# Kernel tuning notes

Hardware: AMD Instinct MI355X
Metric: run time of the kernel (lower is better)

Reference implementation:

```python
import jax, jax.numpy as jnp
import numpy as np

N, E, DIN, DH, DOUT, G = 100000, 1600000, 128, 128, 40, 512


def setup_inputs() -> dict:
    key = jax.random.key(0)
    ks = jax.random.split(key, 8)
    x = jax.random.normal(ks[0], (N, DIN), dtype=jnp.float32)
    src = jax.random.randint(ks[1], (E,), 0, N)
    dst = jax.random.randint(ks[2], (E,), 0, N)
    batch = jnp.sort(jax.random.randint(ks[3], (N,), 0, G))
    W1 = jax.random.normal(ks[4], (DIN, DH), dtype=jnp.float32) * (1.0 / np.sqrt(DIN))
    b1 = jnp.zeros((DH,), dtype=jnp.float32)
    W2 = jax.random.normal(ks[5], (DH, DOUT), dtype=jnp.float32) * (1.0 / np.sqrt(DH))
    b2 = jnp.zeros((DOUT,), dtype=jnp.float32)
    return {"x": x, "src": src, "dst": dst, "batch": batch,
            "W1": W1, "b1": b1, "W2": W2, "b2": b2, "num_graphs": G}


def gcn_conv(h, src, dst, n, W, b):
    # PyG GCNConv: linear transform, then D^-1/2 (A + I) D^-1/2 aggregation.
    h = h @ W  # [n, d_out]
    # degree on destination nodes, including self-loop weight 1
    deg = jax.ops.segment_sum(jnp.ones_like(dst, dtype=h.dtype), dst, num_segments=n) + 1.0
    dinv = jax.lax.rsqrt(deg)  # deg >= 1 so always finite
    coef = dinv[src] * dinv[dst]  # [E]
    agg = jax.ops.segment_sum(h[src] * coef[:, None], dst, num_segments=n)
    agg = agg + h * (dinv * dinv)[:, None]  # self-loop term
    return agg + b


def reference(x, src, dst, batch, W1, b1, W2, b2, num_graphs):
    n = x.shape[0]
    h = jax.nn.relu(gcn_conv(x, src, dst, n, W1, b1))  # dropout = identity (eval mode)
    h = jax.nn.relu(gcn_conv(h, src, dst, n, W2, b2))
    # global mean pool over graphs in the batch
    cnt = jax.ops.segment_sum(jnp.ones((n,), dtype=h.dtype), batch, num_segments=num_graphs)
    pooled = jax.ops.segment_sum(h, batch, num_segments=num_graphs) / jnp.maximum(cnt, 1.0)[:, None]
    return jax.nn.log_softmax(pooled, axis=1)
```

## Files before the change

kernel.cpp:

```cpp
#include <hip/hip_runtime.h>
#include <math.h>


typedef __attribute__((ext_vector_type(4))) float f32x4;
typedef __attribute__((ext_vector_type(8))) short bf16x8;
typedef __attribute__((ext_vector_type(4))) uint uint4v;

constexpr int PAD = 64;
constexpr int CAP = 1536;
constexpr int NBMAX = 1600;

static __device__ __forceinline__ ushort f2bf(float f) {
    union { float f; uint u; } v{f};
    uint r = (v.u + 0x7FFF + ((v.u >> 16) & 1)) >> 16;
    return (ushort)r;
}
static __device__ __forceinline__ float bflo(uint v) {
    union { uint u; float f; } o{v << 16};
    return o.f;
}
static __device__ __forceinline__ float bfhi(uint v) {
    union { uint u; float f; } o{v & 0xffff0000u};
    return o.f;
}
static __device__ __forceinline__ uint packbf(float lo, float hi) {
    return ((uint)f2bf(hi) << 16) | (uint)f2bf(lo);
}

__global__ __launch_bounds__(1024) void k_binhist(
    const int* __restrict__ src, const int* __restrict__ dst, int E, int nbkt,
    int* __restrict__ cur2, int* __restrict__ bins,
    const float* __restrict__ W1, const float* __restrict__ W2,
    ushort* __restrict__ w1t, ushort* __restrict__ w2t, int histB) {
    __shared__ int lc[NBMAX];
    const int bid = blockIdx.x;
    const int t = threadIdx.x;
    if (bid >= histB) {
        int i = (bid - histB) * 1024 + t;
        if (i < 128 * 128) {
            int n = i >> 7, k = i & 127;
            w1t[i] = f2bf(W1[k * 128 + n]);
        } else if (i < 128 * 128 + 48 * 128) {
            int j = i - 128 * 128;
            int n = j >> 7, k = j & 127;
            w2t[j] = (n < 40) ? f2bf(W2[k * 40 + n]) : (ushort)0;
        }
        return;
    }
    for (int b = t; b < nbkt; b += 1024) lc[b] = 0;
    __syncthreads();
    const int elo = (int)(((long long)E * bid) / histB);
    const int ehi = (int)(((long long)E * (bid + 1)) / histB);
    for (int e = elo + t; e < ehi; e += 1024) {
        int d = __builtin_nontemporal_load(&dst[e]);
        atomicAdd(&lc[d >> 6], 1);
    }
    __syncthreads();
    for (int b = t; b < nbkt; b += 1024) {
        int c = lc[b];
        lc[b] = (c > 0) ? atomicAdd(&cur2[b], c) : 0;
    }
    __syncthreads();
    for (int e = elo + t; e < ehi; e += 1024) {
        int d = __builtin_nontemporal_load(&dst[e]);
        int s = __builtin_nontemporal_load(&src[e]);
        int b = d >> 6;
        int pos = atomicAdd(&lc[b], 1);
        if (pos < CAP) bins[(size_t)b * CAP + pos] = ((d & 63) << 17) | s;
    }
}

__global__ __launch_bounds__(256) void k_fillb(const int* __restrict__ cur2,
                                               const int* __restrict__ bins,
                                               int* __restrict__ degi,
                                               int* __restrict__ colidx, int N) {
    __shared__ int lcnt[64];
    const int b = blockIdx.x;
    const int base = b << 6;
    const int t = threadIdx.x;
    if (t < 64) lcnt[t] = 0;
    __syncthreads();
    int cnt = min(cur2[b], CAP);
    for (int i = t; i < cnt; i += 256) {
        int entry = bins[(size_t)b * CAP + i];
        int d = entry >> 17;
        int s = entry & 0x1FFFF;
        int r = atomicAdd(&lcnt[d], 1);
        if (r < PAD) colidx[((base + d) << 6) + r] = s;
    }
    __syncthreads();
    if (t < 64 && base + t < N) degi[base + t] = lcnt[t];
}

template <int NF>
__global__ __launch_bounds__(256) void k_gemm1(const float* __restrict__ A,
                                               const ushort* __restrict__ BT,
                                               const int* __restrict__ degi,
                                               ushort* __restrict__ C, int M,
                                               int NCOLS) {
    __shared__ ushort As[64][136];
    __shared__ ushort Bs[NF * 16][136];
    const int tid = threadIdx.x;
    const int m0 = blockIdx.x * 64;
#pragma unroll
    for (int i = 0; i < 4; i++) {
        int chunk = tid + i * 256;
        int r = chunk >> 4, c8 = chunk & 15;
        float4 v0 = {0.f, 0.f, 0.f, 0.f}, v1 = {0.f, 0.f, 0.f, 0.f};
        if (m0 + r < M) {
            const float* p = &A[(size_t)(m0 + r) * 128 + c8 * 8];
            v0 = *(const float4*)p;
            v1 = *(const float4*)(p + 4);
        }
        ushort o[8];
        o[0] = f2bf(v0.x); o[1] = f2bf(v0.y); o[2] = f2bf(v0.z); o[3] = f2bf(v0.w);
        o[4] = f2bf(v1.x); o[5] = f2bf(v1.y); o[6] = f2bf(v1.z); o[7] = f2bf(v1.w);
        *(float4*)&As[r][c8 * 8] = *(float4*)o;
    }
#pragma unroll
    for (int i = 0; i < NF; i++) {
        int chunk = tid + i * 256;
        int r = chunk >> 4, c = chunk & 15;
        *(float4*)&Bs[r][c * 8] = *(const float4*)&BT[(size_t)r * 128 + c * 8];
    }
    __syncthreads();
    const int wave = tid >> 6, lane = tid & 63;
    const int arow = wave * 16 + (lane & 15);
    const int kgrp = (lane >> 4) * 8;
    f32x4 acc[NF];
#pragma unroll
    for (int i = 0; i < NF; i++) acc[i] = (f32x4){0.f, 0.f, 0.f, 0.f};
#pragma unroll
    for (int kk = 0; kk < 4; kk++) {
        bf16x8 a = *(const bf16x8*)&As[arow][kk * 32 + kgrp];
#pragma unroll
        for (int nf = 0; nf < NF; nf++) {
            bf16x8 b = *(const bf16x8*)&Bs[nf * 16 + (lane & 15)][kk * 32 + kgrp];
            acc[nf] = __builtin_amdgcn_mfma_f32_16x16x32_bf16(a, b, acc[nf], 0, 0, 0);
        }
    }
    const int orow = m0 + wave * 16 + (lane >> 4) * 4;
    float dv[4];
#pragma unroll
    for (int j = 0; j < 4; j++)
        dv[j] = (orow + j < M) ? rsqrtf((float)degi[orow + j] + 1.0f) : 0.f;
#pragma unroll
    for (int nf = 0; nf < NF; nf++) {
        int col = nf * 16 + (lane & 15);
        if (col >= NCOLS) continue;
#pragma unroll
        for (int j = 0; j < 4; j++) {
            int r = orow + j;
            if (r < M) C[(size_t)r * NCOLS + col] = f2bf(dv[j] * acc[nf][j]);
        }
    }
}

template <bool FIRST>
__global__ __launch_bounds__(256) void k_agg128(const ushort* __restrict__ hin,
                                                const int* __restrict__ degi,
                                                const int* __restrict__ colidx,
                                                const float* __restrict__ bias,
                                                ushort* __restrict__ hout, int N) {
    __shared__ int sidx[4][64];
    const int w = threadIdx.x >> 6;
    const int lane = threadIdx.x & 63;
    const int wid = (blockIdx.x * 256 + threadIdx.x) >> 6;
    if (wid >= N) return;
    const int q = lane >> 4;
    const int l16 = lane & 15;
    const uint4v* hu = (const uint4v*)hin;
    const int dg = degi[wid];
    const int cnt = min(dg, PAD);
    const int beg = wid << 6;
    float a0 = 0.f, a1 = 0.f, a2 = 0.f, a3 = 0.f;
    float a4 = 0.f, a5 = 0.f, a6 = 0.f, a7 = 0.f;
    if (lane < cnt) sidx[w][lane] = colidx[beg + lane];
    int i = 0;
    for (; i + 16 <= cnt; i += 16) {
        uint4v v[4];
#pragma unroll
        for (int k = 0; k < 4; k++) {
            v[k] = hu[(size_t)sidx[w][i + 4 * k + q] * 16 + l16];
        }
#pragma unroll
        for (int k = 0; k < 4; k++) {
            a0 += bflo(v[k].x); a1 += bfhi(v[k].x);
            a2 += bflo(v[k].y); a3 += bfhi(v[k].y);
            a4 += bflo(v[k].z); a5 += bfhi(v[k].z);
            a6 += bflo(v[k].w); a7 += bfhi(v[k].w);
        }
    }
    for (; i + q < cnt; i += 4) {
        uint4v vv = hu[(size_t)sidx[w][i + q] * 16 + l16];
        a0 += bflo(vv.x); a1 += bfhi(vv.x);
        a2 += bflo(vv.y); a3 += bfhi(vv.y);
        a4 += bflo(vv.z); a5 += bfhi(vv.z);
        a6 += bflo(vv.w); a7 += bfhi(vv.w);
    }
    a0 += __shfl_xor(a0, 16); a1 += __shfl_xor(a1, 16);
    a2 += __shfl_xor(a2, 16); a3 += __shfl_xor(a3, 16);
    a4 += __shfl_xor(a4, 16); a5 += __shfl_xor(a5, 16);
    a6 += __shfl_xor(a6, 16); a7 += __shfl_xor(a7, 16);
    a0 += __shfl_xor(a0, 32); a1 += __shfl_xor(a1, 32);
    a2 += __shfl_xor(a2, 32); a3 += __shfl_xor(a3, 32);
    a4 += __shfl_xor(a4, 32); a5 += __shfl_xor(a5, 32);
    a6 += __shfl_xor(a6, 32); a7 += __shfl_xor(a7, 32);
    if (lane < 16) {
        float dn = rsqrtf((float)dg + 1.0f);
        uint4v sv = hu[(size_t)wid * 16 + l16];
        a0 += bflo(sv.x); a1 += bfhi(sv.x);
        a2 += bflo(sv.y); a3 += bfhi(sv.y);
        a4 += bflo(sv.z); a5 += bfhi(sv.z);
        a6 += bflo(sv.w); a7 += bfhi(sv.w);
        if (FIRST) {
            float4 b0 = *(const float4*)&bias[l16 * 8];
            float4 b1v = *(const float4*)&bias[l16 * 8 + 4];
            a0 = dn * fmaxf(dn * a0 + b0.x, 0.f);
            a1 = dn * fmaxf(dn * a1 + b0.y, 0.f);
            a2 = dn * fmaxf(dn * a2 + b0.z, 0.f);
            a3 = dn * fmaxf(dn * a3 + b0.w, 0.f);
            a4 = dn * fmaxf(dn * a4 + b1v.x, 0.f);
            a5 = dn * fmaxf(dn * a5 + b1v.y, 0.f);
            a6 = dn * fmaxf(dn * a6 + b1v.z, 0.f);
            a7 = dn * fmaxf(dn * a7 + b1v.w, 0.f);
        } else {
            a0 *= dn; a1 *= dn; a2 *= dn; a3 *= dn;
            a4 *= dn; a5 *= dn; a6 *= dn; a7 *= dn;
        }
        uint4v o;
        o.x = packbf(a0, a1);
        o.y = packbf(a2, a3);
        o.z = packbf(a4, a5);
        o.w = packbf(a6, a7);
        __builtin_nontemporal_store(o, &((uint4v*)hout)[(size_t)wid * 16 + l16]);
    }
}

__global__ __launch_bounds__(256) void k_gemm2_pool(const ushort* __restrict__ A,
                                                    const ushort* __restrict__ BT,
                                                    const float* __restrict__ b2,
                                                    const int* __restrict__ batch,
                                                    float* __restrict__ pooled,
                                                    int M) {
    __shared__ ushort As[64][136];
    __shared__ ushort Bs[48][136];
    __shared__ float smC[64][44];
    __shared__ int sbatch[64];
    const int tid = threadIdx.x;
    const int m0 = blockIdx.x * 64;
#pragma unroll
    for (int i = 0; i < 4; i++) {
        int chunk = tid + i * 256;
        int r = chunk >> 4, c = chunk & 15;
        float4 v = {0.f, 0.f, 0.f, 0.f};
        if (m0 + r < M) v = *(const float4*)&A[((size_t)(m0 + r)) * 128 + c * 8];
        *(float4*)&As[r][c * 8] = v;
    }
#pragma unroll
    for (int i = 0; i < 3; i++) {
        int chunk = tid + i * 256;
        int r = chunk >> 4, c = chunk & 15;
        *(float4*)&Bs[r][c * 8] = *(const float4*)&BT[(size_t)r * 128 + c * 8];
    }
    if (tid < 64) sbatch[tid] = (m0 + tid < M) ? batch[m0 + tid] : -1;
    __syncthreads();
    const int wave = tid >> 6, lane = tid & 63;
    const int arow = wave * 16 + (lane & 15);
    const int kgrp = (lane >> 4) * 8;
    f32x4 acc[3];
#pragma unroll
    for (int i = 0; i < 3; i++) acc[i] = (f32x4){0.f, 0.f, 0.f, 0.f};
#pragma unroll
    for (int kk = 0; kk < 4; kk++) {
        bf16x8 a = *(const bf16x8*)&As[arow][kk * 32 + kgrp];
#pragma unroll
        for (int nf = 0; nf < 3; nf++) {
            bf16x8 b = *(const bf16x8*)&Bs[nf * 16 + (lane & 15)][kk * 32 + kgrp];
            acc[nf] = __builtin_amdgcn_mfma_f32_16x16x32_bf16(a, b, acc[nf], 0, 0, 0);
        }
    }
    const int orowl = wave * 16 + (lane >> 4) * 4;
#pragma unroll
    for (int nf = 0; nf < 3; nf++) {
        int col = nf * 16 + (lane & 15);
        if (col < 40) {
#pragma unroll
            for (int j = 0; j < 4; j++) smC[orowl + j][col] = acc[nf][j];
        }
    }
    __syncthreads();
    int q = tid >> 6, c = tid & 63;
    if (c < 40) {
        float bc = b2[c];
        float run = 0.f;
        int curg = -1;
        for (int r = q * 16; r < q * 16 + 16; ++r) {
            int gid = sbatch[r];
            if (gid < 0) break;
            float v = fmaxf(smC[r][c] + bc, 0.f);
            if (gid != curg) {
                if (curg >= 0) atomicAdd(&pooled[(size_t)curg * 40 + c], run);
                curg = gid;
                run = v;
            } else {
                run += v;
            }
        }
        if (curg >= 0) atomicAdd(&pooled[(size_t)curg * 40 + c], run);
    }
}

__global__ __launch_bounds__(64) void k_finish(const float* __restrict__ pooled,
                                               const int* __restrict__ batch, int N,
                                               int DOUT, float* __restrict__ out) {
    int g = blockIdx.x;
    int c = threadIdx.x;
    int lo = 0, hi = N;
    while (lo < hi) {
        int mid = (lo + hi) >> 1;
        if (batch[mid] < g) lo = mid + 1; else hi = mid;
    }
    int start = lo;
    hi = N;
    int lo2 = lo;
    while (lo2 < hi) {
        int mid = (lo2 + hi) >> 1;
        if (batch[mid] <= g) lo2 = mid + 1; else hi = mid;
    }
    int cnt = lo2 - start;
    float v = (c < DOUT) ? pooled[(size_t)g * DOUT + c] / fmaxf((float)cnt, 1.f) : -1e30f;
    float m = v;
#pragma unroll
    for (int o = 32; o; o >>= 1) m = fmaxf(m, __shfl_xor(m, o));
    float ex = (c < DOUT) ? expf(v - m) : 0.f;
    float s = ex;
#pragma unroll
    for (int o = 32; o; o >>= 1) s += __shfl_xor(s, o);
    if (c < DOUT) out[(size_t)g * DOUT + c] = (v - m) - logf(s);
}

extern "C" void kernel_launch(void* const* d_in, const int* in_sizes, int n_in,
                              void* d_out, int out_size, void* d_ws, size_t ws_size,
                              hipStream_t stream) {
    const float* x = (const float*)d_in[0];
    const int* src = (const int*)d_in[1];
    const int* dst = (const int*)d_in[2];
    const int* batch = (const int*)d_in[3];
    const float* W1 = (const float*)d_in[4];
    const float* b1 = (const float*)d_in[5];
    const float* W2 = (const float*)d_in[6];
    const float* b2 = (const float*)d_in[7];
    float* out = (float*)d_out;

    const int N = in_sizes[3];
    const int E = in_sizes[1];
    const int DOUT = in_sizes[7];
    const int G = out_size / DOUT;
    const int nbkt = (N + 63) >> 6;

    char* ws = (char*)d_ws;
    size_t off = 0;
    auto alloc = [&](size_t bytes) -> char* {
        char* p = ws + off;
        off += (bytes + 255) & ~(size_t)255;
        return p;
    };
    ushort* g1 = (ushort*)alloc((size_t)N * 128 * 2);
    ushort* g2 = (ushort*)alloc((size_t)N * 128 * 2);
    int* colidx = (int*)alloc((size_t)N * PAD * 4);
    int* bins = (int*)alloc((size_t)nbkt * CAP * 4);
    ushort* w1t = (ushort*)alloc(128 * 128 * 2);
    ushort* w2t = (ushort*)alloc(48 * 128 * 2);
    int* degi = (int*)alloc((size_t)N * 4);
    char* z0 = ws + off;
    int* cur2 = (int*)alloc((size_t)nbkt * 4);
    float* pooled = (float*)alloc((size_t)G * DOUT * 4);
    size_t zlen = (size_t)((ws + off) - z0);

    ushort* agg2 = g1;

    hipMemsetAsync(z0, 0, zlen, stream);

    const int TB = 256;
    const int histB = 256;
    const int prepB = (128 * 128 + 48 * 128 + 1023) / 1024;
    k_binhist<<<histB + prepB, 1024, 0, stream>>>(src, dst, E, nbkt, cur2, bins,
                                                  W1, W2, w1t, w2t, histB);
    k_fillb<<<nbkt, TB, 0, stream>>>(cur2, bins, degi, colidx, N);
    k_gemm1<8><<<(N + 63) / 64, TB, 0, stream>>>(x, w1t, degi, g1, N, 128);
    k_agg128<true><<<(N + 3) / 4, TB, 0, stream>>>(g1, degi, colidx, b1, g2, N);
    k_agg128<false><<<(N + 3) / 4, TB, 0, stream>>>(g2, degi, colidx, nullptr, agg2, N);
    k_gemm2_pool<<<(N + 63) / 64, TB, 0, stream>>>(agg2, w2t, b2, batch, pooled, N);
    k_finish<<<G, 64, 0, stream>>>(pooled, batch, N, DOUT, out);
}
```

Before: 218.6 us.

## Fuse layer-1 GEMM into histogram kernel, apply source dinv in aggregation

The first-layer GEMM (x@W1, with W1 transposed to bf16 inside each block) now runs in the same launch as the edge histogram/binning, because the GEMM no longer depends on degrees. The source-side D^-1/2 scaling moves into the first aggregation as a per-edge weight, read from a new dinv array computed in the fill kernel. This drops one kernel launch and the separate W1 prep, and lets the GEMM overlap with the atomic-heavy binning. The cost is extra per-edge dinv gathers and FMAs in aggregation, plus a large shared-memory footprint in the fused kernel that limits occupancy of its histogram blocks.

After: 225.2 us. +3.1%, slower.

```diff
diff --git a/kernel.cpp b/kernel.cpp
--- a/kernel.cpp
+++ b/kernel.cpp
@@ -27,52 +27,110 @@
     return ((uint)f2bf(hi) << 16) | (uint)f2bf(lo);
 }
 
-__global__ __launch_bounds__(1024) void k_binhist(
+__global__ __launch_bounds__(1024) void k_hist_gemm(
     const int* __restrict__ src, const int* __restrict__ dst, int E, int nbkt,
     int* __restrict__ cur2, int* __restrict__ bins,
-    const float* __restrict__ W1, const float* __restrict__ W2,
-    ushort* __restrict__ w1t, ushort* __restrict__ w2t, int histB) {
+    const float* __restrict__ x, const float* __restrict__ W1,
+    ushort* __restrict__ h1, const float* __restrict__ W2,
+    ushort* __restrict__ w2t, int M, int histB, int gemmB) {
+    __shared__ ushort As[128][136];
+    __shared__ ushort Bs[128][136];
     __shared__ int lc[NBMAX];
     const int bid = blockIdx.x;
     const int t = threadIdx.x;
-    if (bid >= histB) {
-        int i = (bid - histB) * 1024 + t;
-        if (i < 128 * 128) {
+    if (bid < histB) {
+        for (int b = t; b < nbkt; b += 1024) lc[b] = 0;
+        __syncthreads();
+        const int elo = (int)(((long long)E * bid) / histB);
+        const int ehi = (int)(((long long)E * (bid + 1)) / histB);
+        for (int e = elo + t; e < ehi; e += 1024) {
+            int d = __builtin_nontemporal_load(&dst[e]);
+            atomicAdd(&lc[d >> 6], 1);
+        }
+        __syncthreads();
+        for (int b = t; b < nbkt; b += 1024) {
+            int c = lc[b];
+            lc[b] = (c > 0) ? atomicAdd(&cur2[b], c) : 0;
+        }
+        __syncthreads();
+        for (int e = elo + t; e < ehi; e += 1024) {
+            int d = __builtin_nontemporal_load(&dst[e]);
+            int s = __builtin_nontemporal_load(&src[e]);
+            int b = d >> 6;
+            int pos = atomicAdd(&lc[b], 1);
+            if (pos < CAP) bins[(size_t)b * CAP + pos] = ((d & 63) << 17) | s;
+        }
+        return;
+    }
+    if (bid >= histB + gemmB) {
+        for (int i = t; i < 48 * 128; i += 1024) {
             int n = i >> 7, k = i & 127;
-            w1t[i] = f2bf(W1[k * 128 + n]);
-        } else if (i < 128 * 128 + 48 * 128) {
-            int j = i - 128 * 128;
-            int n = j >> 7, k = j & 127;
-            w2t[j] = (n < 40) ? f2bf(W2[k * 40 + n]) : (ushort)0;
+            w2t[i] = (n < 40) ? f2bf(W2[k * 40 + n]) : (ushort)0;
         }
         return;
     }
-    for (int b = t; b < nbkt; b += 1024) lc[b] = 0;
+    const int m0 = (bid - histB) * 128;
+#pragma unroll
+    for (int i = 0; i < 2; i++) {
+        int chunk = t + i * 1024;
+        int r = chunk >> 4, c8 = chunk & 15;
+        f32x4 v0 = {0.f, 0.f, 0.f, 0.f}, v1 = {0.f, 0.f, 0.f, 0.f};
+        if (m0 + r < M) {
+            const f32x4* p = (const f32x4*)&x[(size_t)(m0 + r) * 128 + c8 * 8];
+            v0 = __builtin_nontemporal_load(p);
+            v1 = __builtin_nontemporal_load(p + 1);
+        }
+        ushort o[8];
+        o[0] = f2bf(v0.x); o[1] = f2bf(v0.y); o[2] = f2bf(v0.z); o[3] = f2bf(v0.w);
+        o[4] = f2bf(v1.x); o[5] = f2bf(v1.y); o[6] = f2bf(v1.z); o[7] = f2bf(v1.w);
+        *(float4*)&As[r][c8 * 8] = *(float4*)o;
+    }
+#pragma unroll
+    for (int i = 0; i < 4; i++) {
+        int linear = t + i * 1024;
+        int k = linear >> 5;
+        int n4 = (linear & 31) * 4;
+        f32x4 wv = *(const f32x4*)&W1[k * 128 + n4];
+        Bs[n4 + 0][k] = f2bf(wv.x);
+        Bs[n4 + 1][k] = f2bf(wv.y);
+        Bs[n4 + 2][k] = f2bf(wv.z);
+        Bs[n4 + 3][k] = f2bf(wv.w);
+    }
     __syncthreads();
-    const int elo = (int)(((long long)E * bid) / histB);
-    const int ehi = (int)(((long long)E * (bid + 1)) / histB);
-    for (int e = elo + t; e < ehi; e += 1024) {
-        int d = __builtin_nontemporal_load(&dst[e]);
-        atomicAdd(&lc[d >> 6], 1);
-    }
-    __syncthreads();
-    for (int b = t; b < nbkt; b += 1024) {
-        int c = lc[b];
-        lc[b] = (c > 0) ? atomicAdd(&cur2[b], c) : 0;
-    }
-    __syncthreads();
-    for (int e = elo + t; e < ehi; e += 1024) {
-        int d = __builtin_nontemporal_load(&dst[e]);
-        int s = __builtin_nontemporal_load(&src[e]);
-        int b = d >> 6;
-        int pos = atomicAdd(&lc[b], 1);
-        if (pos < CAP) bins[(size_t)b * CAP + pos] = ((d & 63) << 17) | s;
+    const int wave = t >> 6, lane = t & 63;
+    const int rowg = wave & 7, colg = wave >> 3;
+    const int arow = rowg * 16 + (lane & 15);
+    const int kgrp = (lane >> 4) * 8;
+    f32x4 acc[4];
+#pragma unroll
+    for (int i = 0; i < 4; i++) acc[i] = (f32x4){0.f, 0.f, 0.f, 0.f};
+#pragma unroll
+    for (int kk = 0; kk < 4; kk++) {
+        bf16x8 a = *(const bf16x8*)&As[arow][kk * 32 + kgrp];
+#pragma unroll
+        for (int nf = 0; nf < 4; nf++) {
+            bf16x8 b =
+                *(const bf16x8*)&Bs[colg * 64 + nf * 16 + (lane & 15)][kk * 32 + kgrp];
+            acc[nf] = __builtin_amdgcn_mfma_f32_16x16x32_bf16(a, b, acc[nf], 0, 0, 0);
+        }
+    }
+    const int orow = m0 + rowg * 16 + (lane >> 4) * 4;
+#pragma unroll
+    for (int nf = 0; nf < 4; nf++) {
+        int col = colg * 64 + nf * 16 + (lane & 15);
+#pragma unroll
+        for (int j = 0; j < 4; j++) {
+            int r = orow + j;
+            if (r < M)
+                __builtin_nontemporal_store(f2bf(acc[nf][j]), &h1[(size_t)r * 128 + col]);
+        }
     }
 }
 
 __global__ __launch_bounds__(256) void k_fillb(const int* __restrict__ cur2,
                                                const int* __restrict__ bins,
                                                int* __restrict__ degi,
+                                               float* __restrict__ dinv,
                                                int* __restrict__ colidx, int N) {
     __shared__ int lcnt[64];
     const int b = blockIdx.x;
@@ -89,79 +147,102 @@
         if (r < PAD) colidx[((base + d) << 6) + r] = s;
     }
     __syncthreads();
-    if (t < 64 && base + t < N) degi[base + t] = lcnt[t];
-}
-
-template <int NF>
-__global__ __launch_bounds__(256) void k_gemm1(const float* __restrict__ A,
-                                               const ushort* __restrict__ BT,
+    if (t < 64 && base + t < N) {
+        int dg = lcnt[t];
+        degi[base + t] = dg;
+        dinv[base + t] = rsqrtf((float)dg + 1.0f);
+    }
+}
+
+__global__ __launch_bounds__(256) void k_agg1c(const ushort* __restrict__ hin,
                                                const int* __restrict__ degi,
-                                               ushort* __restrict__ C, int M,
-                                               int NCOLS) {
-    __shared__ ushort As[64][136];
-    __shared__ ushort Bs[NF * 16][136];
-    const int tid = threadIdx.x;
-    const int m0 = blockIdx.x * 64;
-#pragma unroll
-    for (int i = 0; i < 4; i++) {
-        int chunk = tid + i * 256;
-        int r = chunk >> 4, c8 = chunk & 15;
-        float4 v0 = {0.f, 0.f, 0.f, 0.f}, v1 = {0.f, 0.f, 0.f, 0.f};
-        if (m0 + r < M) {
-            const float* p = &A[(size_t)(m0 + r) * 128 + c8 * 8];
-            v0 = *(const float4*)p;
-            v1 = *(const float4*)(p + 4);
-        }
-        ushort o[8];
-        o[0] = f2bf(v0.x); o[1] = f2bf(v0.y); o[2] = f2bf(v0.z); o[3] = f2bf(v0.w);
-        o[4] = f2bf(v1.x); o[5] = f2bf(v1.y); o[6] = f2bf(v1.z); o[7] = f2bf(v1.w);
-        *(float4*)&As[r][c8 * 8] = *(float4*)o;
-    }
-#pragma unroll
-    for (int i = 0; i < NF; i++) {
-        int chunk = tid + i * 256;
-        int r = chunk >> 4, c = chunk & 15;
-        *(float4*)&Bs[r][c * 8] = *(const float4*)&BT[(size_t)r * 128 + c * 8];
-    }
-    __syncthreads();
-    const int wave = tid >> 6, lane = tid & 63;
-    const int arow = wave * 16 + (lane & 15);
-    const int kgrp = (lane >> 4) * 8;
-    f32x4 acc[NF];
-#pragma unroll
-    for (int i = 0; i < NF; i++) acc[i] = (f32x4){0.f, 0.f, 0.f, 0.f};
-#pragma unroll
-    for (int kk = 0; kk < 4; kk++) {
-        bf16x8 a = *(const bf16x8*)&As[arow][kk * 32 + kgrp];
-#pragma unroll
-        for (int nf = 0; nf < NF; nf++) {
-            bf16x8 b = *(const bf16x8*)&Bs[nf * 16 + (lane & 15)][kk * 32 + kgrp];
-            acc[nf] = __builtin_amdgcn_mfma_f32_16x16x32_bf16(a, b, acc[nf], 0, 0, 0);
-        }
-    }
-    const int orow = m0 + wave * 16 + (lane >> 4) * 4;
-    float dv[4];
-#pragma unroll
-    for (int j = 0; j < 4; j++)
-        dv[j] = (orow + j < M) ? rsqrtf((float)degi[orow + j] + 1.0f) : 0.f;
-#pragma unroll
-    for (int nf = 0; nf < NF; nf++) {
-        int col = nf * 16 + (lane & 15);
-        if (col >= NCOLS) continue;
-#pragma unroll
-        for (int j = 0; j < 4; j++) {
-            int r = orow + j;
-            if (r < M) C[(size_t)r * NCOLS + col] = f2bf(dv[j] * acc[nf][j]);
-        }
-    }
-}
-
-template <bool FIRST>
-__global__ __launch_bounds__(256) void k_agg128(const ushort* __restrict__ hin,
-                                                const int* __restrict__ degi,
-                                                const int* __restrict__ colidx,
-                                                const float* __restrict__ bias,
-                                                ushort* __restrict__ hout, int N) {
+                                               const float* __restrict__ dinv,
+                                               const int* __restrict__ colidx,
+                                               const float* __restrict__ bias,
+                                               ushort* __restrict__ hout, int N) {
+    __shared__ int sidx[4][64];
+    __shared__ float sdinv[4][64];
+    const int w = threadIdx.x >> 6;
+    const int lane = threadIdx.x & 63;
+    const int wid = (blockIdx.x * 256 + threadIdx.x) >> 6;
+    if (wid >= N) return;
+    const int q = lane >> 4;
+    const int l16 = lane & 15;
+    const uint4v* hu = (const uint4v*)hin;
+    const int dg = degi[wid];
+    const int cnt = min(dg, PAD);
+    const int beg = wid << 6;
+    float a0 = 0.f, a1 = 0.f, a2 = 0.f, a3 = 0.f;
+    float a4 = 0.f, a5 = 0.f, a6 = 0.f, a7 = 0.f;
+    if (lane < cnt) {
+        int myidx = colidx[beg + lane];
+        sidx[w][lane] = myidx;
+        sdinv[w][lane] = dinv[myidx];
+    }
+    int i = 0;
+    for (; i + 16 <= cnt; i += 16) {
+        uint4v v[4];
+        float cw[4];
+#pragma unroll
+        for (int k = 0; k < 4; k++) {
+            int sl = i + 4 * k + q;
+            cw[k] = sdinv[w][sl];
+            v[k] = hu[(size_t)sidx[w][sl] * 16 + l16];
+        }
+#pragma unroll
+        for (int k = 0; k < 4; k++) {
+            a0 += cw[k] * bflo(v[k].x); a1 += cw[k] * bfhi(v[k].x);
+            a2 += cw[k] * bflo(v[k].y); a3 += cw[k] * bfhi(v[k].y);
+            a4 += cw[k] * bflo(v[k].z); a5 += cw[k] * bfhi(v[k].z);
+            a6 += cw[k] * bflo(v[k].w); a7 += cw[k] * bfhi(v[k].w);
+        }
+    }
+    for (; i + q < cnt; i += 4) {
+        float cw = sdinv[w][i + q];
+        uint4v vv = hu[(size_t)sidx[w][i + q] * 16 + l16];
+        a0 += cw * bflo(vv.x); a1 += cw * bfhi(vv.x);
+        a2 += cw * bflo(vv.y); a3 += cw * bfhi(vv.y);
+        a4 += cw * bflo(vv.z); a5 += cw * bfhi(vv.z);
+        a6 += cw * bflo(vv.w); a7 += cw * bfhi(vv.w);
+    }
+    a0 += __shfl_xor(a0, 16); a1 += __shfl_xor(a1, 16);
+    a2 += __shfl_xor(a2, 16); a3 += __shfl_xor(a3, 16);
+    a4 += __shfl_xor(a4, 16); a5 += __shfl_xor(a5, 16);
+    a6 += __shfl_xor(a6, 16); a7 += __shfl_xor(a7, 16);
+    a0 += __shfl_xor(a0, 32); a1 += __shfl_xor(a1, 32);
+    a2 += __shfl_xor(a2, 32); a3 += __shfl_xor(a3, 32);
+    a4 += __shfl_xor(a4, 32); a5 += __shfl_xor(a5, 32);
+    a6 += __shfl_xor(a6, 32); a7 += __shfl_xor(a7, 32);
+    if (lane < 16) {
+        float dn = rsqrtf((float)dg + 1.0f);
+        uint4v sv = hu[(size_t)wid * 16 + l16];
+        a0 += dn * bflo(sv.x); a1 += dn * bfhi(sv.x);
+        a2 += dn * bflo(sv.y); a3 += dn * bfhi(sv.y);
+        a4 += dn * bflo(sv.z); a5 += dn * bfhi(sv.z);
+        a6 += dn * bflo(sv.w); a7 += dn * bfhi(sv.w);
+        float4 b0 = *(const float4*)&bias[l16 * 8];
+        float4 b1v = *(const float4*)&bias[l16 * 8 + 4];
+        a0 = dn * fmaxf(dn * a0 + b0.x, 0.f);
+        a1 = dn * fmaxf(dn * a1 + b0.y, 0.f);
+        a2 = dn * fmaxf(dn * a2 + b0.z, 0.f);
+        a3 = dn * fmaxf(dn * a3 + b0.w, 0.f);
+        a4 = dn * fmaxf(dn * a4 + b1v.x, 0.f);
+        a5 = dn * fmaxf(dn * a5 + b1v.y, 0.f);
+        a6 = dn * fmaxf(dn * a6 + b1v.z, 0.f);
+        a7 = dn * fmaxf(dn * a7 + b1v.w, 0.f);
+        uint4v o;
+        o.x = packbf(a0, a1);
+        o.y = packbf(a2, a3);
+        o.z = packbf(a4, a5);
+        o.w = packbf(a6, a7);
+        __builtin_nontemporal_store(o, &((uint4v*)hout)[(size_t)wid * 16 + l16]);
+    }
+}
+
+__global__ __launch_bounds__(256) void k_agg2p(const ushort* __restrict__ hin,
+                                               const int* __restrict__ degi,
+                                               const int* __restrict__ colidx,
+                                               ushort* __restrict__ hout, int N) {
     __shared__ int sidx[4][64];
     const int w = threadIdx.x >> 6;
     const int lane = threadIdx.x & 63;
@@ -213,21 +294,8 @@
         a2 += bflo(sv.y); a3 += bfhi(sv.y);
         a4 += bflo(sv.z); a5 += bfhi(sv.z);
         a6 += bflo(sv.w); a7 += bfhi(sv.w);
-        if (FIRST) {
-            float4 b0 = *(const float4*)&bias[l16 * 8];
-            float4 b1v = *(const float4*)&bias[l16 * 8 + 4];
-            a0 = dn * fmaxf(dn * a0 + b0.x, 0.f);
-            a1 = dn * fmaxf(dn * a1 + b0.y, 0.f);
-            a2 = dn * fmaxf(dn * a2 + b0.z, 0.f);
-            a3 = dn * fmaxf(dn * a3 + b0.w, 0.f);
-            a4 = dn * fmaxf(dn * a4 + b1v.x, 0.f);
-            a5 = dn * fmaxf(dn * a5 + b1v.y, 0.f);
-            a6 = dn * fmaxf(dn * a6 + b1v.z, 0.f);
-            a7 = dn * fmaxf(dn * a7 + b1v.w, 0.f);
-        } else {
-            a0 *= dn; a1 *= dn; a2 *= dn; a3 *= dn;
-            a4 *= dn; a5 *= dn; a6 *= dn; a7 *= dn;
-        }
+        a0 *= dn; a1 *= dn; a2 *= dn; a3 *= dn;
+        a4 *= dn; a5 *= dn; a6 *= dn; a7 *= dn;
         uint4v o;
         o.x = packbf(a0, a1);
         o.y = packbf(a2, a3);
@@ -366,31 +434,30 @@
         off += (bytes + 255) & ~(size_t)255;
         return p;
     };
-    ushort* g1 = (ushort*)alloc((size_t)N * 128 * 2);
+    ushort* h1 = (ushort*)alloc((size_t)N * 128 * 2);
     ushort* g2 = (ushort*)alloc((size_t)N * 128 * 2);
     int* colidx = (int*)alloc((size_t)N * PAD * 4);
     int* bins = (int*)alloc((size_t)nbkt * CAP * 4);
-    ushort* w1t = (ushort*)alloc(128 * 128 * 2);
     ushort* w2t = (ushort*)alloc(48 * 128 * 2);
     int* degi = (int*)alloc((size_t)N * 4);
+    float* dinv = (float*)alloc((size_t)N * 4);
     char* z0 = ws + off;
     int* cur2 = (int*)alloc((size_t)nbkt * 4);
     float* pooled = (float*)alloc((size_t)G * DOUT * 4);
     size_t zlen = (size_t)((ws + off) - z0);
 
-    ushort* agg2 = g1;
+    ushort* agg2 = h1;
 
     hipMemsetAsync(z0, 0, zlen, stream);
 
     const int TB = 256;
     const int histB = 256;
-    const int prepB = (128 * 128 + 48 * 128 + 1023) / 1024;
-    k_binhist<<<histB + prepB, 1024, 0, stream>>>(src, dst, E, nbkt, cur2, bins,
-                                                  W1, W2, w1t, w2t, histB);
-    k_fillb<<<nbkt, TB, 0, stream>>>(cur2, bins, degi, colidx, N);
-    k_gemm1<8><<<(N + 63) / 64, TB, 0, stream>>>(x, w1t, degi, g1, N, 128);
-    k_agg128<true><<<(N + 3) / 4, TB, 0, stream>>>(g1, degi, colidx, b1, g2, N);
-    k_agg128<false><<<(N + 3) / 4, TB, 0, stream>>>(g2, degi, colidx, nullptr, agg2, N);
+    const int gemmB = (N + 127) / 128;
+    k_hist_gemm<<<histB + gemmB + 1, 1024, 0, stream>>>(
+        src, dst, E, nbkt, cur2, bins, x, W1, h1, W2, w2t, N, histB, gemmB);
+    k_fillb<<<nbkt, TB, 0, stream>>>(cur2, bins, degi, dinv, colidx, N);
+    k_agg1c<<<(N + 3) / 4, TB, 0, stream>>>(h1, degi, dinv, colidx, b1, g2, N);
+    k_agg2p<<<(N + 3) / 4, TB, 0, stream>>>(g2, degi, colidx, agg2, N);
     k_gemm2_pool<<<(N + 63) / 64, TB, 0, stream>>>(agg2, w2t, b2, batch, pooled, N);
     k_finish<<<G, 64, 0, stream>>>(pooled, batch, N, DOUT, out);
 }
```

## Transform before aggregating in layer two and pool with a per-graph reduction

Applied to the files above, without the earlier changes.

Layer two now applies the 128→40 weight (padded to 64 columns) before neighbour aggregation, not after. The edge gather therefore reads 128-byte bf16 rows instead of 256-byte rows, which targets the memory-bound gather cost. A new k_agg40 kernel aggregates and applies bias and ReLU, writing fp32 activations. A per-graph k_pool kernel then sums rows and computes log-softmax, replacing the atomic pooling. The trade-off is an extra N×40 fp32 intermediate that must be written and read back.

Result: no change. 214.8 us (-1.7%).

```diff
diff --git a/kernel.cpp b/kernel.cpp
--- a/kernel.cpp
+++ b/kernel.cpp
@@ -5,6 +5,7 @@
 typedef __attribute__((ext_vector_type(4))) float f32x4;
 typedef __attribute__((ext_vector_type(8))) short bf16x8;
 typedef __attribute__((ext_vector_type(4))) uint uint4v;
+typedef __attribute__((ext_vector_type(2))) uint uint2v;
 
 constexpr int PAD = 64;
 constexpr int CAP = 1536;
@@ -40,7 +41,7 @@
         if (i < 128 * 128) {
             int n = i >> 7, k = i & 127;
             w1t[i] = f2bf(W1[k * 128 + n]);
-        } else if (i < 128 * 128 + 48 * 128) {
+        } else if (i < 128 * 128 + 64 * 128) {
             int j = i - 128 * 128;
             int n = j >> 7, k = j & 127;
             w2t[j] = (n < 40) ? f2bf(W2[k * 40 + n]) : (ushort)0;
@@ -156,7 +157,6 @@
     }
 }
 
-template <bool FIRST>
 __global__ __launch_bounds__(256) void k_agg128(const ushort* __restrict__ hin,
                                                 const int* __restrict__ degi,
                                                 const int* __restrict__ colidx,
@@ -213,21 +213,16 @@
         a2 += bflo(sv.y); a3 += bfhi(sv.y);
         a4 += bflo(sv.z); a5 += bfhi(sv.z);
         a6 += bflo(sv.w); a7 += bfhi(sv.w);
-        if (FIRST) {
-            float4 b0 = *(const float4*)&bias[l16 * 8];
-            float4 b1v = *(const float4*)&bias[l16 * 8 + 4];
-            a0 = dn * fmaxf(dn * a0 + b0.x, 0.f);
-            a1 = dn * fmaxf(dn * a1 + b0.y, 0.f);
-            a2 = dn * fmaxf(dn * a2 + b0.z, 0.f);
-            a3 = dn * fmaxf(dn * a3 + b0.w, 0.f);
-            a4 = dn * fmaxf(dn * a4 + b1v.x, 0.f);
-            a5 = dn * fmaxf(dn * a5 + b1v.y, 0.f);
-            a6 = dn * fmaxf(dn * a6 + b1v.z, 0.f);
-            a7 = dn * fmaxf(dn * a7 + b1v.w, 0.f);
-        } else {
-            a0 *= dn; a1 *= dn; a2 *= dn; a3 *= dn;
-            a4 *= dn; a5 *= dn; a6 *= dn; a7 *= dn;
-        }
+        float4 b0 = *(const float4*)&bias[l16 * 8];
+        float4 b1v = *(const float4*)&bias[l16 * 8 + 4];
+        a0 = dn * fmaxf(dn * a0 + b0.x, 0.f);
+        a1 = dn * fmaxf(dn * a1 + b0.y, 0.f);
+        a2 = dn * fmaxf(dn * a2 + b0.z, 0.f);
+        a3 = dn * fmaxf(dn * a3 + b0.w, 0.f);
+        a4 = dn * fmaxf(dn * a4 + b1v.x, 0.f);
+        a5 = dn * fmaxf(dn * a5 + b1v.y, 0.f);
+        a6 = dn * fmaxf(dn * a6 + b1v.z, 0.f);
+        a7 = dn * fmaxf(dn * a7 + b1v.w, 0.f);
         uint4v o;
         o.x = packbf(a0, a1);
         o.y = packbf(a2, a3);
@@ -237,16 +232,11 @@
     }
 }
 
-__global__ __launch_bounds__(256) void k_gemm2_pool(const ushort* __restrict__ A,
-                                                    const ushort* __restrict__ BT,
-                                                    const float* __restrict__ b2,
-                                                    const int* __restrict__ batch,
-                                                    float* __restrict__ pooled,
-                                                    int M) {
+__global__ __launch_bounds__(256) void k_gemm_p(const ushort* __restrict__ A,
+                                                const ushort* __restrict__ BT,
+                                                ushort* __restrict__ P, int M) {
     __shared__ ushort As[64][136];
-    __shared__ ushort Bs[48][136];
-    __shared__ float smC[64][44];
-    __shared__ int sbatch[64];
+    __shared__ ushort Bs[64][136];
     const int tid = threadIdx.x;
     const int m0 = blockIdx.x * 64;
 #pragma unroll
@@ -258,64 +248,100 @@
         *(float4*)&As[r][c * 8] = v;
     }
 #pragma unroll
-    for (int i = 0; i < 3; i++) {
+    for (int i = 0; i < 4; i++) {
         int chunk = tid + i * 256;
         int r = chunk >> 4, c = chunk & 15;
         *(float4*)&Bs[r][c * 8] = *(const float4*)&BT[(size_t)r * 128 + c * 8];
     }
-    if (tid < 64) sbatch[tid] = (m0 + tid < M) ? batch[m0 + tid] : -1;
     __syncthreads();
     const int wave = tid >> 6, lane = tid & 63;
     const int arow = wave * 16 + (lane & 15);
     const int kgrp = (lane >> 4) * 8;
-    f32x4 acc[3];
-#pragma unroll
-    for (int i = 0; i < 3; i++) acc[i] = (f32x4){0.f, 0.f, 0.f, 0.f};
+    f32x4 acc[4];
+#pragma unroll
+    for (int i = 0; i < 4; i++) acc[i] = (f32x4){0.f, 0.f, 0.f, 0.f};
 #pragma unroll
     for (int kk = 0; kk < 4; kk++) {
         bf16x8 a = *(const bf16x8*)&As[arow][kk * 32 + kgrp];
 #pragma unroll
-        for (int nf = 0; nf < 3; nf++) {
+        for (int nf = 0; nf < 4; nf++) {
             bf16x8 b = *(const bf16x8*)&Bs[nf * 16 + (lane & 15)][kk * 32 + kgrp];
             acc[nf] = __builtin_amdgcn_mfma_f32_16x16x32_bf16(a, b, acc[nf], 0, 0, 0);
         }
     }
-    const int orowl = wave * 16 + (lane >> 4) * 4;
-#pragma unroll
-    for (int nf = 0; nf < 3; nf++) {
+    const int orow = m0 + wave * 16 + (lane >> 4) * 4;
+#pragma unroll
+    for (int nf = 0; nf < 4; nf++) {
         int col = nf * 16 + (lane & 15);
-        if (col < 40) {
-#pragma unroll
-            for (int j = 0; j < 4; j++) smC[orowl + j][col] = acc[nf][j];
-        }
-    }
-    __syncthreads();
-    int q = tid >> 6, c = tid & 63;
-    if (c < 40) {
-        float bc = b2[c];
-        float run = 0.f;
-        int curg = -1;
-        for (int r = q * 16; r < q * 16 + 16; ++r) {
-            int gid = sbatch[r];
-            if (gid < 0) break;
-            float v = fmaxf(smC[r][c] + bc, 0.f);
-            if (gid != curg) {
-                if (curg >= 0) atomicAdd(&pooled[(size_t)curg * 40 + c], run);
-                curg = gid;
-                run = v;
-            } else {
-                run += v;
-            }
-        }
-        if (curg >= 0) atomicAdd(&pooled[(size_t)curg * 40 + c], run);
-    }
-}
-
-__global__ __launch_bounds__(64) void k_finish(const float* __restrict__ pooled,
-                                               const int* __restrict__ batch, int N,
-                                               int DOUT, float* __restrict__ out) {
+#pragma unroll
+        for (int j = 0; j < 4; j++) {
+            int r = orow + j;
+            if (r < M)
+                __builtin_nontemporal_store(f2bf(acc[nf][j]), &P[(size_t)r * 64 + col]);
+        }
+    }
+}
+
+__global__ __launch_bounds__(256) void k_agg40(const ushort* __restrict__ p,
+                                               const int* __restrict__ degi,
+                                               const int* __restrict__ colidx,
+                                               const float* __restrict__ b2,
+                                               float* __restrict__ h2a, int N) {
+    __shared__ int sidx[4][64];
+    const int w = threadIdx.x >> 6;
+    const int lane = threadIdx.x & 63;
+    const int wid = (blockIdx.x * 256 + threadIdx.x) >> 6;
+    if (wid >= N) return;
+    const int q = lane >> 4;
+    const int l16 = lane & 15;
+    const uint2v* hu = (const uint2v*)p;
+    const int dg = degi[wid];
+    const int cnt = min(dg, PAD);
+    const int beg = wid << 6;
+    float a0 = 0.f, a1 = 0.f, a2 = 0.f, a3 = 0.f;
+    if (lane < cnt) sidx[w][lane] = colidx[beg + lane];
+    int i = 0;
+    for (; i + 16 <= cnt; i += 16) {
+        uint2v v[4];
+#pragma unroll
+        for (int k = 0; k < 4; k++) {
+            v[k] = hu[(size_t)sidx[w][i + 4 * k + q] * 16 + l16];
+        }
+#pragma unroll
+        for (int k = 0; k < 4; k++) {
+            a0 += bflo(v[k].x); a1 += bfhi(v[k].x);
+            a2 += bflo(v[k].y); a3 += bfhi(v[k].y);
+        }
+    }
+    for (; i + q < cnt; i += 4) {
+        uint2v vv = hu[(size_t)sidx[w][i + q] * 16 + l16];
+        a0 += bflo(vv.x); a1 += bfhi(vv.x);
+        a2 += bflo(vv.y); a3 += bfhi(vv.y);
+    }
+    a0 += __shfl_xor(a0, 16); a1 += __shfl_xor(a1, 16);
+    a2 += __shfl_xor(a2, 16); a3 += __shfl_xor(a3, 16);
+    a0 += __shfl_xor(a0, 32); a1 += __shfl_xor(a1, 32);
+    a2 += __shfl_xor(a2, 32); a3 += __shfl_xor(a3, 32);
+    if (lane < 16 && l16 < 10) {
+        float dn = rsqrtf((float)dg + 1.0f);
+        uint2v sv = hu[(size_t)wid * 16 + l16];
+        a0 += bflo(sv.x); a1 += bfhi(sv.x);
+        a2 += bflo(sv.y); a3 += bfhi(sv.y);
+        float4 bb = *(const float4*)&b2[l16 * 4];
+        float4 o;
+        o.x = fmaxf(dn * a0 + bb.x, 0.f);
+        o.y = fmaxf(dn * a1 + bb.y, 0.f);
+        o.z = fmaxf(dn * a2 + bb.z, 0.f);
+        o.w = fmaxf(dn * a3 + bb.w, 0.f);
+        *(float4*)&h2a[(size_t)wid * 40 + l16 * 4] = o;
+    }
+}
+
+__global__ __launch_bounds__(256) void k_pool(const float* __restrict__ h2a,
+                                              const int* __restrict__ batch, int N,
+                                              int DOUT, float* __restrict__ out) {
     int g = blockIdx.x;
-    int c = threadIdx.x;
+    int t = threadIdx.x;
     int lo = 0, hi = N;
     while (lo < hi) {
         int mid = (lo + hi) >> 1;
@@ -323,21 +349,33 @@
     }
     int start = lo;
     hi = N;
-    int lo2 = lo;
-    while (lo2 < hi) {
-        int mid = (lo2 + hi) >> 1;
-        if (batch[mid] <= g) lo2 = mid + 1; else hi = mid;
-    }
-    int cnt = lo2 - start;
-    float v = (c < DOUT) ? pooled[(size_t)g * DOUT + c] / fmaxf((float)cnt, 1.f) : -1e30f;
-    float m = v;
-#pragma unroll
-    for (int o = 32; o; o >>= 1) m = fmaxf(m, __shfl_xor(m, o));
-    float ex = (c < DOUT) ? expf(v - m) : 0.f;
-    float s = ex;
-#pragma unroll
-    for (int o = 32; o; o >>= 1) s += __shfl_xor(s, o);
-    if (c < DOUT) out[(size_t)g * DOUT + c] = (v - m) - logf(s);
+    while (lo < hi) {
+        int mid = (lo + hi) >> 1;
+        if (batch[mid] <= g) lo = mid + 1; else hi = mid;
+    }
+    int end = lo;
+    int cnt = end - start;
+    int c = t & 63, rr = t >> 6;
+    float acc = 0.f;
+    if (c < DOUT) {
+        for (int i = start + rr; i < end; i += 4) acc += h2a[(size_t)i * DOUT + c];
+    }
+    __shared__ float sm[4][64];
+    sm[rr][c] = acc;
+    __syncthreads();
+    if (t < 64) {
+        float v = (c < DOUT)
+                      ? (sm[0][c] + sm[1][c] + sm[2][c] + sm[3][c]) / fmaxf((float)cnt, 1.f)
+                      : -1e30f;
+        float m = v;
+#pragma unroll
+        for (int o = 32; o; o >>= 1) m = fmaxf(m, __shfl_xor(m, o));
+        float ex = (c < DOUT) ? expf(v - m) : 0.f;
+        float s = ex;
+#pragma unroll
+        for (int o = 32; o; o >>= 1) s += __shfl_xor(s, o);
+        if (c < DOUT) out[g * DOUT + c] = (v - m) - logf(s);
+    }
 }
 
 extern "C" void kernel_launch(void* const* d_in, const int* in_sizes, int n_in,
@@ -371,26 +409,26 @@
     int* colidx = (int*)alloc((size_t)N * PAD * 4);
     int* bins = (int*)alloc((size_t)nbkt * CAP * 4);
     ushort* w1t = (ushort*)alloc(128 * 128 * 2);
-    ushort* w2t = (ushort*)alloc(48 * 128 * 2);
+    ushort* w2t = (ushort*)alloc(64 * 128 * 2);
     int* degi = (int*)alloc((size_t)N * 4);
+    float* h2a = (float*)alloc((size_t)N * 40 * 4);
     char* z0 = ws + off;
     int* cur2 = (int*)alloc((size_t)nbkt * 4);
-    float* pooled = (float*)alloc((size_t)G * DOUT * 4);
     size_t zlen = (size_t)((ws + off) - z0);
 
-    ushort* agg2 = g1;
+    ushort* p = g1;
 
     hipMemsetAsync(z0, 0, zlen, stream);
 
     const int TB = 256;
     const int histB = 256;
-    const int prepB = (128 * 128 + 48 * 128 + 1023) / 1024;
+    const int prepB = (128 * 128 + 64 * 128 + 1023) / 1024;
     k_binhist<<<histB + prepB, 1024, 0, stream>>>(src, dst, E, nbkt, cur2, bins,
                                                   W1, W2, w1t, w2t, histB);
     k_fillb<<<nbkt, TB, 0, stream>>>(cur2, bins, degi, colidx, N);
     k_gemm1<8><<<(N + 63) / 64, TB, 0, stream>>>(x, w1t, degi, g1, N, 128);
-    k_agg128<true><<<(N + 3) / 4, TB, 0, stream>>>(g1, degi, colidx, b1, g2, N);
-    k_agg128<false><<<(N + 3) / 4, TB, 0, stream>>>(g2, degi, colidx, nullptr, agg2, N);
-    k_gemm2_pool<<<(N + 63) / 64, TB, 0, stream>>>(agg2, w2t, b2, batch, pooled, N);
-    k_finish<<<G, 64, 0, stream>>>(pooled, batch, N, DOUT, out);
-}
+    k_agg128<<<(N + 3) / 4, TB, 0, stream>>>(g1, degi, colidx, b1, g2, N);
+    k_gemm_p<<<(N + 63) / 64, TB, 0, stream>>>(g2, w2t, p, N);
+    k_agg40<<<(N + 3) / 4, TB, 0, stream>>>(p, degi, colidx, b2, h2a, N);
+    k_pool<<<G, TB, 0, stream>>>(h2a, batch, N, DOUT, out);
+}
```
